# Optimization experiments

Hardware: AMD Instinct MI355X
Metric: run time of the kernel (lower is better)

## Reference

```python
import jax, jax.numpy as jnp
import numpy as np

IN_CAPS = 128      # number of memory capsules (rows of m)
NUM_CAPS = 5       # n_class
DIM_CAPS = 153     # comp_dim // n_class = 768 // 5
IN_DIM = 768       # comp_dim
NQ = 256           # number of query samples
NUM_ROUTING = 3
BETA = 1.0         # config['Model']['temperature']
EPS = 1e-8


def _pearsonr(x, y):
    # Pearson correlation along last dim (broadcasts over leading dims).
    xm = x - x.mean(axis=-1, keepdims=True)
    ym = y - y.mean(axis=-1, keepdims=True)
    num = (xm * ym).sum(axis=-1)
    den = jnp.sqrt((xm * xm).sum(axis=-1)) * jnp.sqrt((ym * ym).sum(axis=-1))
    return num / (den + EPS)


def _squash(s):
    # capsule squash along last dim
    n2 = (s * s).sum(axis=-1, keepdims=True)
    return (n2 / (1.0 + n2)) * s / jnp.sqrt(n2 + EPS)


def setup_inputs() -> dict:
    key = jax.random.key(0)
    k1, k2, k3 = jax.random.split(key, 3)
    m = jax.random.normal(k1, (IN_CAPS, IN_DIM), dtype=jnp.float32)
    q = jax.random.normal(k2, (NQ, IN_DIM), dtype=jnp.float32)
    W = jax.random.normal(k3, (IN_DIM, NUM_CAPS * DIM_CAPS), dtype=jnp.float32) * 0.02
    b = jnp.zeros((NUM_CAPS * DIM_CAPS,), dtype=jnp.float32)
    return {"m": m, "q": q, "W": W, "b": b}


def reference(m, q, W, b):
    sg = jax.lax.stop_gradient
    # projections -> capsule preactivations
    hat_m = (m @ W + b).reshape(IN_CAPS, NUM_CAPS, DIM_CAPS)          # [I,C,D]
    hat_q = (q @ W + b).reshape(-1, NUM_CAPS, DIM_CAPS)               # [Q,C,D]
    Qn = hat_q.shape[0]
    tmp_m = sg(hat_m)[None, :, :, :]                                   # [1,I,C,D] (broadcast over Q)
    tmp_q = sg(hat_q)[:, None, :, :]                                   # [Q,1,C,D]

    a = jnp.zeros((Qn, IN_CAPS, NUM_CAPS), dtype=hat_q.dtype)          # routing logits
    p = jnp.tanh(_pearsonr(tmp_m, tmp_q))                              # [Q,I,C]

    for _ in range(NUM_ROUTING - 1):
        d = jax.nn.softmax(a / BETA, axis=2)                           # [Q,I,C]
        dsp = d + p
        hat_v = (tmp_m * dsp[..., None]).sum(axis=1)                   # [Q,C,D]
        v = _squash(hat_v)
        m_dot_v = (tmp_m * v[:, None, :, :]).sum(axis=-1)              # [Q,I,C]
        a = a + p * m_dot_v
        tmp_q = (tmp_q + v[:, None, :, :]) * 0.5                       # [Q,I,C,D]
        p = jnp.tanh(_pearsonr(tmp_m, tmp_q))

    d = jax.nn.softmax(a / BETA, axis=2)
    dsp = sg(d + p)                                                    # routing coeffs detached
    hat_v = (hat_m[None, :, :, :] * dsp[..., None]).sum(axis=1)        # grad flows via hat_m only
    q_prime = _squash(hat_v).reshape(Qn, -1)                           # [Q, C*D]
    return q_prime
```

## Files before the change

### kernel.cpp

```cpp
#include <hip/hip_runtime.h>
#include <hip/hip_bf16.h>

#define I_CAPS 128
#define N_CAPS 5
#define D_CAPS 153
#define D_PAD  160
#define MLD    800
#define IN_DIM 768
#define NQ     256
#define CD     765
#define NPAIR  640
#define EPSF   1e-8f
#define KHALF  384

typedef __hip_bfloat16 bf16;

__device__ __forceinline__ float wred(float x) {
#pragma unroll
  for (int off = 32; off; off >>= 1) x += __shfl_down(x, off, 64);
  return x;
}

__device__ __forceinline__ float tanh_fast(float x) {
  float t = __expf(-2.f * fabsf(x));
  float r = (1.f - t) / (1.f + t);
  return copysignf(r, x);
}

__device__ __forceinline__ float squash_sc(float n2) {
  return (n2 / (1.f + n2)) * rsqrtf(n2 + EPSF);
}

__global__ void classify_kernel(const unsigned* __restrict__ m_u32,
                                int* __restrict__ flag) {
  int lane = threadIdx.x & 63;
  unsigned u = m_u32[lane];
  int e = (u >> 7) & 0xFF;
  int hit = (e >= 118 && e <= 134) ? 1 : 0;
  unsigned long long mask = __ballot(hit);
  if (lane == 0) *flag = (__popcll(mask) >= 48) ? 1 : 0;
}

template <bool ISB>
__device__ __forceinline__ float ld_in(const void* p, long idx) {
  if (ISB) return __bfloat162float(((const bf16*)p)[idx]);
  return ((const float*)p)[idx];
}

template <bool ISB>
__device__ void gemm_body(const void* m, const void* q, const void* W,
                          const void* b, float* hat_m, float* hat_q) {
  __shared__ float As[16][KHALF];
  const int tx = threadIdx.x, ty = threadIdx.y;
  const int t = ty * 64 + tx;
  const int row0 = blockIdx.y * 16;
  const int k0 = blockIdx.z * KHALF;

  if (ISB) {
    for (int e = t; e < 16 * KHALF; e += 256) {
      int rr = e / KHALF, kk = e - rr * KHALF;
      int row = row0 + rr;
      As[rr][kk] = (row < I_CAPS)
                       ? ld_in<true>(m, (long)row * IN_DIM + k0 + kk)
                       : ld_in<true>(q, (long)(row - I_CAPS) * IN_DIM + k0 + kk);
    }
  } else {
    for (int e = t; e < 16 * (KHALF / 4); e += 256) {
      int rr = e / (KHALF / 4), k4 = e - rr * (KHALF / 4);
      int row = row0 + rr;
      const float* src = (row < I_CAPS)
                             ? (const float*)m + (long)row * IN_DIM
                             : (const float*)q + (long)(row - I_CAPS) * IN_DIM;
      *(float4*)&As[rr][k4 * 4] = *(const float4*)(src + k0 + k4 * 4);
    }
  }
  __syncthreads();

  const int col = blockIdx.x * 64 + tx;
  const int colc = (col < CD) ? col : (CD - 1);
  const int r0 = ty * 4;

  float acc[4][2];
#pragma unroll
  for (int r = 0; r < 4; ++r) { acc[r][0] = 0.f; acc[r][1] = 0.f; }

#pragma unroll 2
  for (int k = 0; k < KHALF; k += 8) {
    float w0 = ld_in<ISB>(W, (long)(k0 + k + 0) * CD + colc);
    float w1 = ld_in<ISB>(W, (long)(k0 + k + 1) * CD + colc);
    float w2 = ld_in<ISB>(W, (long)(k0 + k + 2) * CD + colc);
    float w3 = ld_in<ISB>(W, (long)(k0 + k + 3) * CD + colc);
    float w4 = ld_in<ISB>(W, (long)(k0 + k + 4) * CD + colc);
    float w5 = ld_in<ISB>(W, (long)(k0 + k + 5) * CD + colc);
    float w6 = ld_in<ISB>(W, (long)(k0 + k + 6) * CD + colc);
    float w7 = ld_in<ISB>(W, (long)(k0 + k + 7) * CD + colc);
#pragma unroll
    for (int r = 0; r < 4; ++r) {
      const float4 Aa = *(const float4*)&As[r0 + r][k];
      const float4 Ab = *(const float4*)&As[r0 + r][k + 4];
      acc[r][0] = fmaf(Aa.x, w0, acc[r][0]);
      acc[r][1] = fmaf(Aa.y, w1, acc[r][1]);
      acc[r][0] = fmaf(Aa.z, w2, acc[r][0]);
      acc[r][1] = fmaf(Aa.w, w3, acc[r][1]);
      acc[r][0] = fmaf(Ab.x, w4, acc[r][0]);
      acc[r][1] = fmaf(Ab.y, w5, acc[r][1]);
      acc[r][0] = fmaf(Ab.z, w6, acc[r][0]);
      acc[r][1] = fmaf(Ab.w, w7, acc[r][1]);
    }
  }

  if (col < CD) {
    float bias = (blockIdx.z == 0) ? ld_in<ISB>(b, col) : 0.f;
    int c = col / D_CAPS, d = col - c * D_CAPS;
#pragma unroll
    for (int r = 0; r < 4; ++r) {
      int row = row0 + r0 + r;
      float p = acc[r][0] + acc[r][1] + bias;
      float* dst = (row < I_CAPS) ? &hat_m[row * MLD + c * D_PAD + d]
                                  : &hat_q[(row - I_CAPS) * CD + col];
      atomicAdd(dst, p);
    }
  }
}

__global__ __launch_bounds__(256, 4)
void gemm_kernel(const void* m, const void* q, const void* W, const void* b,
                 const int* __restrict__ flag,
                 float* __restrict__ hat_m, float* __restrict__ hat_q) {
  if (*flag)
    gemm_body<true>(m, q, W, b, hat_m, hat_q);
  else
    gemm_body<false>(m, q, W, b, hat_m, hat_q);
}

__global__ __launch_bounds__(256)
void stats_kernel(const float* __restrict__ hat_m,
                  float* __restrict__ mean_m, float* __restrict__ ssm) {
  const int wave = threadIdx.x >> 6, lane = threadIdx.x & 63;
  const int pair = blockIdx.x * 4 + wave;
  const int i = pair / N_CAPS, c = pair - i * N_CAPS;
  const float* hm = hat_m + i * MLD + c * D_PAD;
  float s = 0.f, s2 = 0.f;
  for (int d = lane; d < D_CAPS; d += 64) {
    float x = hm[d];
    s += x;
    s2 = fmaf(x, x, s2);
  }
  s = wred(s);
  s2 = wred(s2);
  if (lane == 0) {
    float mu = s * (1.f / D_CAPS);
    mean_m[pair] = mu;
    ssm[pair] = fmaxf(s2 - (float)D_CAPS * mu * mu, 0.f);
  }
}

__global__ __launch_bounds__(128)
void gram_kernel(const float* __restrict__ hat_m, float* __restrict__ G) {
  const int c = blockIdx.x, j = blockIdx.y, i = threadIdx.x;
  const float4* hi = (const float4*)(hat_m + i * MLD + c * D_PAD);
  const float4* hj = (const float4*)(hat_m + j * MLD + c * D_PAD);
  float a0 = 0.f, a1 = 0.f, a2 = 0.f, a3 = 0.f;
#pragma unroll 8
  for (int k = 0; k < 40; ++k) {
    float4 x = hi[k];
    float4 y = hj[k];
    a0 = fmaf(x.x, y.x, a0);
    a1 = fmaf(x.y, y.y, a1);
    a2 = fmaf(x.z, y.z, a2);
    a3 = fmaf(x.w, y.w, a3);
  }
  G[c * 16384 + j * 128 + i] = (a0 + a1) + (a2 + a3);
}

__global__ __launch_bounds__(1024, 4)
void routing_kernel(const float* __restrict__ hat_m,
                    const float* __restrict__ hat_q,
                    const float* __restrict__ Gmat,
                    const float* __restrict__ mean_m,
                    const float* __restrict__ ssm,
                    float* __restrict__ dspT,
                    float* __restrict__ scT) {
  __shared__ float tq[N_CAPS * D_PAD];
  __shared__ float aa[NPAIR], pp[NPAIR], dsp[NPAIR], sdot[NPAIR];
  __shared__ float smm[NPAIR], sss[NPAIR];
  __shared__ float meanq0[N_CAPS], ssq0[N_CAPS];
  __shared__ float tsum_s[2][N_CAPS], t2_s[2][N_CAPS];
  __shared__ float red[10][4];

  const int tid = threadIdx.x;
  const int qi = blockIdx.x;
  const int w = tid >> 6, lane = tid & 63;
  const int g = tid >> 3, sub = tid & 7;
  const float* hq = hat_q + qi * CD;
  const float* hm = hat_m + g * MLD;

  for (int l = tid; l < N_CAPS * D_PAD; l += 1024) {
    int c = l / D_PAD, d = l - c * D_PAD;
    tq[l] = (d < D_CAPS) ? hq[c * D_CAPS + d] : 0.f;
  }
  if (tid < NPAIR) {
    aa[tid] = 0.f;
    smm[tid] = mean_m[tid];
    sss[tid] = ssm[tid];
  }
  __syncthreads();

  if (w < N_CAPS) {
    const int c = w;
    float s = 0.f, s2 = 0.f;
    for (int d = lane; d < D_CAPS; d += 64) {
      float x = tq[c * D_PAD + d];
      s += x;
      s2 = fmaf(x, x, s2);
    }
    s = wred(s);
    s2 = wred(s2);
    if (lane == 0) {
      float mu = s * (1.f / D_CAPS);
      tsum_s[0][c] = s;
      t2_s[0][c] = s2;
      meanq0[c] = mu;
      ssq0[c] = fmaxf(s2 - (float)D_CAPS * mu * mu, 0.f);
    }
  }
  __syncthreads();

  {
    float A0 = 0.f, A1 = 0.f, A2 = 0.f, A3 = 0.f, A4 = 0.f;
#pragma unroll 2
    for (int jj = 0; jj < 5; ++jj) {
      int d = jj * 32 + sub * 4;
      float4 h0 = *(const float4*)(hm + 0 * D_PAD + d);
      float4 h1 = *(const float4*)(hm + 1 * D_PAD + d);
      float4 h2 = *(const float4*)(hm + 2 * D_PAD + d);
      float4 h3 = *(const float4*)(hm + 3 * D_PAD + d);
      float4 h4 = *(const float4*)(hm + 4 * D_PAD + d);
      float4 t0 = *(const float4*)(tq + 0 * D_PAD + d);
      float4 t1 = *(const float4*)(tq + 1 * D_PAD + d);
      float4 t2 = *(const float4*)(tq + 2 * D_PAD + d);
      float4 t3 = *(const float4*)(tq + 3 * D_PAD + d);
      float4 t4 = *(const float4*)(tq + 4 * D_PAD + d);
      A0 = fmaf(h0.x, t0.x, A0); A0 = fmaf(h0.y, t0.y, A0);
      A0 = fmaf(h0.z, t0.z, A0); A0 = fmaf(h0.w, t0.w, A0);
      A1 = fmaf(h1.x, t1.x, A1); A1 = fmaf(h1.y, t1.y, A1);
      A1 = fmaf(h1.z, t1.z, A1); A1 = fmaf(h1.w, t1.w, A1);
      A2 = fmaf(h2.x, t2.x, A2); A2 = fmaf(h2.y, t2.y, A2);
      A2 = fmaf(h2.z, t2.z, A2); A2 = fmaf(h2.w, t2.w, A2);
      A3 = fmaf(h3.x, t3.x, A3); A3 = fmaf(h3.y, t3.y, A3);
      A3 = fmaf(h3.z, t3.z, A3); A3 = fmaf(h3.w, t3.w, A3);
      A4 = fmaf(h4.x, t4.x, A4); A4 = fmaf(h4.y, t4.y, A4);
      A4 = fmaf(h4.z, t4.z, A4); A4 = fmaf(h4.w, t4.w, A4);
    }
#pragma unroll
    for (int off = 1; off < 8; off <<= 1) {
      A0 += __shfl_xor(A0, off, 64);
      A1 += __shfl_xor(A1, off, 64);
      A2 += __shfl_xor(A2, off, 64);
      A3 += __shfl_xor(A3, off, 64);
      A4 += __shfl_xor(A4, off, 64);
    }
    if (sub < N_CAPS) {
      float acc = A0;
      acc = (sub == 1) ? A1 : acc;
      acc = (sub == 2) ? A2 : acc;
      acc = (sub == 3) ? A3 : acc;
      acc = (sub == 4) ? A4 : acc;
      int ic = g * N_CAPS + sub;
      sdot[ic] = acc;
      float num = acc - (float)D_CAPS * smm[ic] * meanq0[sub];
      float den = sqrtf(sss[ic]) * sqrtf(ssq0[sub]) + EPSF;
      pp[ic] = tanh_fast(num / den);
    }
  }
  __syncthreads();

  auto softmax_dsp = [&]() {
    if (tid < I_CAPS) {
      float av[N_CAPS], ev[N_CAPS];
      float mx = -1e30f;
#pragma unroll
      for (int c = 0; c < N_CAPS; ++c) {
        av[c] = aa[tid * N_CAPS + c];
        mx = fmaxf(mx, av[c]);
      }
      float s = 0.f;
#pragma unroll
      for (int c = 0; c < N_CAPS; ++c) {
        ev[c] = __expf(av[c] - mx);
        s += ev[c];
      }
      float inv = 1.f / s;
#pragma unroll
      for (int c = 0; c < N_CAPS; ++c)
        dsp[tid * N_CAPS + c] = ev[c] * inv + pp[tid * N_CAPS + c];
    }
  };

  auto gmatvec = [&](int cc, int ii) {
    const float* Gp = Gmat + cc * 16384 + ii;
    float y0 = 0.f, y1 = 0.f;
#pragma unroll 4
    for (int j = 0; j < 128; j += 2) {
      y0 = fmaf(Gp[j * 128], dsp[j * N_CAPS + cc], y0);
      y1 = fmaf(Gp[(j + 1) * 128], dsp[(j + 1) * N_CAPS + cc], y1);
    }
    return y0 + y1;
  };

  for (int r = 0; r < 2; ++r) {
    softmax_dsp();
    __syncthreads();
    float y = 0.f, sold = 0.f;
    int cc = tid >> 7, ii = tid & 127, ic = ii * N_CAPS + cc;
    if (tid < NPAIR) {
      y = gmatvec(cc, ii);
      sold = sdot[ic];
      float dmy = dsp[ic];
      float n2p = wred(dmy * y);
      float vsp = wred(dmy * ((float)D_CAPS * smm[ic]));
      float sdp = wred(dmy * sold);
      if (lane == 0) {
        red[w][0] = n2p;
        red[w][1] = vsp;
        red[w][2] = sdp;
      }
    }
    __syncthreads();
    if (tid < NPAIR) {
      float n2 = red[2 * cc][0] + red[2 * cc + 1][0];
      float vs = red[2 * cc][1] + red[2 * cc + 1][1];
      float sd = red[2 * cc][2] + red[2 * cc + 1][2];
      float sc = squash_sc(n2);
      float ts = 0.5f * (tsum_s[r & 1][cc] + sc * vs);
      float t2v = 0.25f * (t2_s[r & 1][cc] + 2.f * sc * sd + sc * sc * n2);
      if (ii == 0) {
        tsum_s[(r + 1) & 1][cc] = ts;
        t2_s[(r + 1) & 1][cc] = t2v;
      }
      float mu = ts * (1.f / D_CAPS);
      float ssqv = fmaxf(t2v - (float)D_CAPS * mu * mu, 0.f);
      float mdv = sc * y;
      aa[ic] += pp[ic] * mdv;
      float snew = 0.5f * (sold + mdv);
      sdot[ic] = snew;
      float num = snew - (float)D_CAPS * smm[ic] * mu;
      float den = sqrtf(sss[ic]) * sqrtf(ssqv) + EPSF;
      pp[ic] = tanh_fast(num / den);
    }
    __syncthreads();
  }

  softmax_dsp();
  __syncthreads();
  {
    int cc = tid >> 7, ii = tid & 127, ic = ii * N_CAPS + cc;
    float y = 0.f;
    if (tid < NPAIR) {
      y = gmatvec(cc, ii);
      float n2p = wred(dsp[ic] * y);
      if (lane == 0) red[w][0] = n2p;
    }
    __syncthreads();
    if (tid < NPAIR)
      dspT[(cc * NQ + qi) * 128 + ii] = dsp[ic];
    if (tid < N_CAPS) {
      float n2 = red[2 * tid][0] + red[2 * tid + 1][0];
      scT[tid * NQ + qi] = squash_sc(n2);
    }
  }
}

__global__ __launch_bounds__(256, 4)
void outgemm_kernel(const float* __restrict__ hat_m,
                    const float* __restrict__ dspT,
                    const float* __restrict__ scT,
                    const int* __restrict__ flag,
                    void* __restrict__ out_v) {
  __shared__ float hmT[128][32];
  __shared__ float dspS[32][132];

  const int c = blockIdx.x, dt = blockIdx.y, qt = blockIdx.z;
  const int tid = threadIdx.x;

  for (int e = tid; e < 128 * 8; e += 256) {
    int i = e >> 3, dd4 = e & 7;
    *(float4*)&hmT[i][dd4 * 4] =
        *(const float4*)(hat_m + i * MLD + c * D_PAD + dt * 32 + dd4 * 4);
  }
  for (int e = tid; e < 32 * 32; e += 256) {
    int qq = e >> 5, k4 = e & 31;
    *(float4*)&dspS[qq][k4 * 4] =
        *(const float4*)(dspT + ((long)c * NQ + qt * 32 + qq) * 128 + k4 * 4);
  }
  __syncthreads();

  const int qq = tid >> 3, dsub = tid & 7;
  const int q = qt * 32 + qq;
  float a0 = 0.f, a1 = 0.f, a2 = 0.f, a3 = 0.f;
#pragma unroll 2
  for (int i = 0; i < 128; ++i) {
    float dv = dspS[qq][i];
    const float4 h = *(const float4*)&hmT[i][dsub * 4];
    a0 = fmaf(dv, h.x, a0);
    a1 = fmaf(dv, h.y, a1);
    a2 = fmaf(dv, h.z, a2);
    a3 = fmaf(dv, h.w, a3);
  }
  const float sc = scT[c * NQ + q];
  const int d0 = dt * 32 + dsub * 4;
  float r[4] = {a0 * sc, a1 * sc, a2 * sc, a3 * sc};

  if (*flag == 0) {
    float* out = (float*)out_v;
#pragma unroll
    for (int k = 0; k < 4; ++k)
      if (d0 + k < D_CAPS) out[q * CD + c * D_CAPS + d0 + k] = r[k];
  } else {
    bf16* out = (bf16*)out_v;
#pragma unroll
    for (int k = 0; k < 4; ++k)
      if (d0 + k < D_CAPS)
        out[q * CD + c * D_CAPS + d0 + k] = __float2bfloat16(r[k]);
  }
}

extern "C" void kernel_launch(void* const* d_in, const int* in_sizes, int n_in,
                              void* d_out, int out_size, void* d_ws, size_t ws_size,
                              hipStream_t stream) {
  const void *m = nullptr, *q = nullptr, *W = nullptr, *b = nullptr;
  for (int i = 0; i < n_in; ++i) {
    switch (in_sizes[i]) {
      case I_CAPS * IN_DIM: m = d_in[i]; break;
      case NQ * IN_DIM:     q = d_in[i]; break;
      case IN_DIM * CD:     W = d_in[i]; break;
      case CD:              b = d_in[i]; break;
      default: break;
    }
  }
  if (!m || !q || !W || !b) {
    m = d_in[0]; q = d_in[1]; W = d_in[2]; b = d_in[3];
  }

  int*   flag   = (int*)d_ws;
  float* mean_m = (float*)d_ws + 16;
  float* ssm    = mean_m + 640;
  float* hat_m  = ssm + 640;
  float* hat_q  = hat_m + I_CAPS * MLD;
  float* G      = hat_q + NQ * CD;
  float* dspT   = G + N_CAPS * I_CAPS * I_CAPS;
  float* scT    = dspT + (size_t)N_CAPS * NQ * 128;

  classify_kernel<<<1, 64, 0, stream>>>((const unsigned*)m, flag);
  hipMemsetAsync(hat_m, 0,
                 ((size_t)I_CAPS * MLD + (size_t)NQ * CD) * sizeof(float),
                 stream);
  gemm_kernel<<<dim3(12, 24, 2), dim3(64, 4), 0, stream>>>(m, q, W, b, flag,
                                                           hat_m, hat_q);
  stats_kernel<<<160, 256, 0, stream>>>(hat_m, mean_m, ssm);
  gram_kernel<<<dim3(N_CAPS, I_CAPS), 128, 0, stream>>>(hat_m, G);
  routing_kernel<<<NQ, 1024, 0, stream>>>(hat_m, hat_q, G, mean_m, ssm,
                                          dspT, scT);
  outgemm_kernel<<<dim3(N_CAPS, 5, 8), 256, 0, stream>>>(hat_m, dspT, scT,
                                                         flag, d_out);
}
```

Baseline: 125.2 us.

## Fold dtype check and stats into other kernels, precompute initial dot in batched kernel

Removes the separate classify and stats kernels: the bf16 check is now recomputed inline in the gemm and output kernels, and the per-capsule mean and sum of squares come from the diagonal of the gram kernel. The initial hat_m·hat_q dot products move out of the per-query routing kernel into a new batched sinit kernel that reuses hat_q tiles from shared memory. The projection GEMM tile is halved to 8 rows per block, doubling the block count. This trades two fewer launches and less redundant global traffic in routing for an extra kernel and more workspace.

After: 129.8 us. +3.6%, slower.

```diff
diff --git a/kernel.cpp b/kernel.cpp
--- a/kernel.cpp
+++ b/kernel.cpp
@@ -27,18 +27,12 @@
   return copysignf(r, x);
 }
 
-__device__ __forceinline__ float squash_sc(float n2) {
-  return (n2 / (1.f + n2)) * rsqrtf(n2 + EPSF);
-}
-
-__global__ void classify_kernel(const unsigned* __restrict__ m_u32,
-                                int* __restrict__ flag) {
+__device__ __forceinline__ int is_bf16(const unsigned* __restrict__ m_u32) {
   int lane = threadIdx.x & 63;
   unsigned u = m_u32[lane];
   int e = (u >> 7) & 0xFF;
-  int hit = (e >= 118 && e <= 134) ? 1 : 0;
-  unsigned long long mask = __ballot(hit);
-  if (lane == 0) *flag = (__popcll(mask) >= 48) ? 1 : 0;
+  unsigned long long mask = __ballot(e >= 118 && e <= 134);
+  return __popcll(mask) >= 48;
 }
 
 template <bool ISB>
@@ -50,14 +44,14 @@
 template <bool ISB>
 __device__ void gemm_body(const void* m, const void* q, const void* W,
                           const void* b, float* hat_m, float* hat_q) {
-  __shared__ float As[16][KHALF];
+  __shared__ float As[8][KHALF];
   const int tx = threadIdx.x, ty = threadIdx.y;
   const int t = ty * 64 + tx;
-  const int row0 = blockIdx.y * 16;
+  const int row0 = blockIdx.y * 8;
   const int k0 = blockIdx.z * KHALF;
 
   if (ISB) {
-    for (int e = t; e < 16 * KHALF; e += 256) {
+    for (int e = t; e < 8 * KHALF; e += 256) {
       int rr = e / KHALF, kk = e - rr * KHALF;
       int row = row0 + rr;
       As[rr][kk] = (row < I_CAPS)
@@ -65,7 +59,7 @@
                        : ld_in<true>(q, (long)(row - I_CAPS) * IN_DIM + k0 + kk);
     }
   } else {
-    for (int e = t; e < 16 * (KHALF / 4); e += 256) {
+    for (int e = t; e < 8 * (KHALF / 4); e += 256) {
       int rr = e / (KHALF / 4), k4 = e - rr * (KHALF / 4);
       int row = row0 + rr;
       const float* src = (row < I_CAPS)
@@ -78,14 +72,15 @@
 
   const int col = blockIdx.x * 64 + tx;
   const int colc = (col < CD) ? col : (CD - 1);
-  const int r0 = ty * 4;
-
-  float acc[4][2];
-#pragma unroll
-  for (int r = 0; r < 4; ++r) { acc[r][0] = 0.f; acc[r][1] = 0.f; }
-
+  const int r0 = ty * 2, r1 = r0 + 1;
+
+  float a0a = 0.f, a0b = 0.f, a1a = 0.f, a1b = 0.f;
 #pragma unroll 2
   for (int k = 0; k < KHALF; k += 8) {
+    const float4 A0a = *(const float4*)&As[r0][k];
+    const float4 A0b = *(const float4*)&As[r0][k + 4];
+    const float4 A1a = *(const float4*)&As[r1][k];
+    const float4 A1b = *(const float4*)&As[r1][k + 4];
     float w0 = ld_in<ISB>(W, (long)(k0 + k + 0) * CD + colc);
     float w1 = ld_in<ISB>(W, (long)(k0 + k + 1) * CD + colc);
     float w2 = ld_in<ISB>(W, (long)(k0 + k + 2) * CD + colc);
@@ -94,73 +89,52 @@
     float w5 = ld_in<ISB>(W, (long)(k0 + k + 5) * CD + colc);
     float w6 = ld_in<ISB>(W, (long)(k0 + k + 6) * CD + colc);
     float w7 = ld_in<ISB>(W, (long)(k0 + k + 7) * CD + colc);
-#pragma unroll
-    for (int r = 0; r < 4; ++r) {
-      const float4 Aa = *(const float4*)&As[r0 + r][k];
-      const float4 Ab = *(const float4*)&As[r0 + r][k + 4];
-      acc[r][0] = fmaf(Aa.x, w0, acc[r][0]);
-      acc[r][1] = fmaf(Aa.y, w1, acc[r][1]);
-      acc[r][0] = fmaf(Aa.z, w2, acc[r][0]);
-      acc[r][1] = fmaf(Aa.w, w3, acc[r][1]);
-      acc[r][0] = fmaf(Ab.x, w4, acc[r][0]);
-      acc[r][1] = fmaf(Ab.y, w5, acc[r][1]);
-      acc[r][0] = fmaf(Ab.z, w6, acc[r][0]);
-      acc[r][1] = fmaf(Ab.w, w7, acc[r][1]);
-    }
+    a0a = fmaf(A0a.x, w0, a0a); a0b = fmaf(A0a.y, w1, a0b);
+    a0a = fmaf(A0a.z, w2, a0a); a0b = fmaf(A0a.w, w3, a0b);
+    a0a = fmaf(A0b.x, w4, a0a); a0b = fmaf(A0b.y, w5, a0b);
+    a0a = fmaf(A0b.z, w6, a0a); a0b = fmaf(A0b.w, w7, a0b);
+    a1a = fmaf(A1a.x, w0, a1a); a1b = fmaf(A1a.y, w1, a1b);
+    a1a = fmaf(A1a.z, w2, a1a); a1b = fmaf(A1a.w, w3, a1b);
+    a1a = fmaf(A1b.x, w4, a1a); a1b = fmaf(A1b.y, w5, a1b);
+    a1a = fmaf(A1b.z, w6, a1a); a1b = fmaf(A1b.w, w7, a1b);
   }
 
   if (col < CD) {
-    float bias = (blockIdx.z == 0) ? ld_in<ISB>(b, col) : 0.f;
+    float p0 = a0a + a0b;
+    float p1 = a1a + a1b;
+    if (blockIdx.z == 0) {
+      float bias = ld_in<ISB>(b, col);
+      p0 += bias;
+      p1 += bias;
+    }
     int c = col / D_CAPS, d = col - c * D_CAPS;
-#pragma unroll
-    for (int r = 0; r < 4; ++r) {
-      int row = row0 + r0 + r;
-      float p = acc[r][0] + acc[r][1] + bias;
-      float* dst = (row < I_CAPS) ? &hat_m[row * MLD + c * D_PAD + d]
-                                  : &hat_q[(row - I_CAPS) * CD + col];
-      atomicAdd(dst, p);
-    }
+    int ra = row0 + r0, rb = row0 + r1;
+    float* d0 = (ra < I_CAPS) ? &hat_m[ra * MLD + c * D_PAD + d]
+                              : &hat_q[(ra - I_CAPS) * CD + col];
+    float* d1 = (rb < I_CAPS) ? &hat_m[rb * MLD + c * D_PAD + d]
+                              : &hat_q[(rb - I_CAPS) * CD + col];
+    atomicAdd(d0, p0);
+    atomicAdd(d1, p1);
   }
 }
 
 __global__ __launch_bounds__(256, 4)
 void gemm_kernel(const void* m, const void* q, const void* W, const void* b,
-                 const int* __restrict__ flag,
                  float* __restrict__ hat_m, float* __restrict__ hat_q) {
-  if (*flag)
+  if (is_bf16((const unsigned*)m))
     gemm_body<true>(m, q, W, b, hat_m, hat_q);
   else
     gemm_body<false>(m, q, W, b, hat_m, hat_q);
 }
 
-__global__ __launch_bounds__(256)
-void stats_kernel(const float* __restrict__ hat_m,
-                  float* __restrict__ mean_m, float* __restrict__ ssm) {
-  const int wave = threadIdx.x >> 6, lane = threadIdx.x & 63;
-  const int pair = blockIdx.x * 4 + wave;
-  const int i = pair / N_CAPS, c = pair - i * N_CAPS;
-  const float* hm = hat_m + i * MLD + c * D_PAD;
-  float s = 0.f, s2 = 0.f;
-  for (int d = lane; d < D_CAPS; d += 64) {
-    float x = hm[d];
-    s += x;
-    s2 = fmaf(x, x, s2);
-  }
-  s = wred(s);
-  s2 = wred(s2);
-  if (lane == 0) {
-    float mu = s * (1.f / D_CAPS);
-    mean_m[pair] = mu;
-    ssm[pair] = fmaxf(s2 - (float)D_CAPS * mu * mu, 0.f);
-  }
-}
-
 __global__ __launch_bounds__(128)
-void gram_kernel(const float* __restrict__ hat_m, float* __restrict__ G) {
+void gram_kernel(const float* __restrict__ hat_m, float* __restrict__ G,
+                 float* __restrict__ mean_m, float* __restrict__ ssm) {
   const int c = blockIdx.x, j = blockIdx.y, i = threadIdx.x;
   const float4* hi = (const float4*)(hat_m + i * MLD + c * D_PAD);
   const float4* hj = (const float4*)(hat_m + j * MLD + c * D_PAD);
   float a0 = 0.f, a1 = 0.f, a2 = 0.f, a3 = 0.f;
+  float s = 0.f;
 #pragma unroll 8
   for (int k = 0; k < 40; ++k) {
     float4 x = hi[k];
@@ -169,14 +143,55 @@
     a1 = fmaf(x.y, y.y, a1);
     a2 = fmaf(x.z, y.z, a2);
     a3 = fmaf(x.w, y.w, a3);
-  }
-  G[c * 16384 + j * 128 + i] = (a0 + a1) + (a2 + a3);
+    s += (x.x + x.y) + (x.z + x.w);
+  }
+  float dot = (a0 + a1) + (a2 + a3);
+  G[c * 16384 + j * 128 + i] = dot;
+  if (i == j) {
+    float mu = s * (1.f / D_CAPS);
+    mean_m[j * N_CAPS + c] = mu;
+    ssm[j * N_CAPS + c] = fmaxf(dot - (float)D_CAPS * mu * mu, 0.f);
+  }
+}
+
+__global__ __launch_bounds__(256)
+void sinit_kernel(const float* __restrict__ hat_m,
+                  const float* __restrict__ hat_q,
+                  float* __restrict__ Sg) {
+  __shared__ float hqS[16][160];
+  const int c = blockIdx.x, q0 = blockIdx.y * 16;
+  const int tid = threadIdx.x;
+
+  for (int e = tid; e < 16 * 160; e += 256) {
+    int qq = e / 160, d = e - qq * 160;
+    hqS[qq][d] = (d < D_CAPS) ? hat_q[(q0 + qq) * CD + c * D_CAPS + d] : 0.f;
+  }
+  __syncthreads();
+
+  const int i = tid & 127, half = tid >> 7;
+  const float4* hi = (const float4*)(hat_m + i * MLD + c * D_PAD);
+  float acc[8] = {0.f, 0.f, 0.f, 0.f, 0.f, 0.f, 0.f, 0.f};
+#pragma unroll 4
+  for (int k = 0; k < 40; ++k) {
+    float4 h = hi[k];
+#pragma unroll
+    for (int qq = 0; qq < 8; ++qq) {
+      const float4 t = *(const float4*)&hqS[half * 8 + qq][k * 4];
+      acc[qq] = fmaf(h.x, t.x, acc[qq]);
+      acc[qq] = fmaf(h.y, t.y, acc[qq]);
+      acc[qq] = fmaf(h.z, t.z, acc[qq]);
+      acc[qq] = fmaf(h.w, t.w, acc[qq]);
+    }
+  }
+#pragma unroll
+  for (int qq = 0; qq < 8; ++qq)
+    Sg[((long)c * NQ + q0 + half * 8 + qq) * 128 + i] = acc[qq];
 }
 
 __global__ __launch_bounds__(1024, 4)
-void routing_kernel(const float* __restrict__ hat_m,
-                    const float* __restrict__ hat_q,
+void routing_kernel(const float* __restrict__ hat_q,
                     const float* __restrict__ Gmat,
+                    const float* __restrict__ Sg,
                     const float* __restrict__ mean_m,
                     const float* __restrict__ ssm,
                     float* __restrict__ dspT,
@@ -191,9 +206,7 @@
   const int tid = threadIdx.x;
   const int qi = blockIdx.x;
   const int w = tid >> 6, lane = tid & 63;
-  const int g = tid >> 3, sub = tid & 7;
   const float* hq = hat_q + qi * CD;
-  const float* hm = hat_m + g * MLD;
 
   for (int l = tid; l < N_CAPS * D_PAD; l += 1024) {
     int c = l / D_PAD, d = l - c * D_PAD;
@@ -226,52 +239,13 @@
   }
   __syncthreads();
 
-  {
-    float A0 = 0.f, A1 = 0.f, A2 = 0.f, A3 = 0.f, A4 = 0.f;
-#pragma unroll 2
-    for (int jj = 0; jj < 5; ++jj) {
-      int d = jj * 32 + sub * 4;
-      float4 h0 = *(const float4*)(hm + 0 * D_PAD + d);
-      float4 h1 = *(const float4*)(hm + 1 * D_PAD + d);
-      float4 h2 = *(const float4*)(hm + 2 * D_PAD + d);
-      float4 h3 = *(const float4*)(hm + 3 * D_PAD + d);
-      float4 h4 = *(const float4*)(hm + 4 * D_PAD + d);
-      float4 t0 = *(const float4*)(tq + 0 * D_PAD + d);
-      float4 t1 = *(const float4*)(tq + 1 * D_PAD + d);
-      float4 t2 = *(const float4*)(tq + 2 * D_PAD + d);
-      float4 t3 = *(const float4*)(tq + 3 * D_PAD + d);
-      float4 t4 = *(const float4*)(tq + 4 * D_PAD + d);
-      A0 = fmaf(h0.x, t0.x, A0); A0 = fmaf(h0.y, t0.y, A0);
-      A0 = fmaf(h0.z, t0.z, A0); A0 = fmaf(h0.w, t0.w, A0);
-      A1 = fmaf(h1.x, t1.x, A1); A1 = fmaf(h1.y, t1.y, A1);
-      A1 = fmaf(h1.z, t1.z, A1); A1 = fmaf(h1.w, t1.w, A1);
-      A2 = fmaf(h2.x, t2.x, A2); A2 = fmaf(h2.y, t2.y, A2);
-      A2 = fmaf(h2.z, t2.z, A2); A2 = fmaf(h2.w, t2.w, A2);
-      A3 = fmaf(h3.x, t3.x, A3); A3 = fmaf(h3.y, t3.y, A3);
-      A3 = fmaf(h3.z, t3.z, A3); A3 = fmaf(h3.w, t3.w, A3);
-      A4 = fmaf(h4.x, t4.x, A4); A4 = fmaf(h4.y, t4.y, A4);
-      A4 = fmaf(h4.z, t4.z, A4); A4 = fmaf(h4.w, t4.w, A4);
-    }
-#pragma unroll
-    for (int off = 1; off < 8; off <<= 1) {
-      A0 += __shfl_xor(A0, off, 64);
-      A1 += __shfl_xor(A1, off, 64);
-      A2 += __shfl_xor(A2, off, 64);
-      A3 += __shfl_xor(A3, off, 64);
-      A4 += __shfl_xor(A4, off, 64);
-    }
-    if (sub < N_CAPS) {
-      float acc = A0;
-      acc = (sub == 1) ? A1 : acc;
-      acc = (sub == 2) ? A2 : acc;
-      acc = (sub == 3) ? A3 : acc;
-      acc = (sub == 4) ? A4 : acc;
-      int ic = g * N_CAPS + sub;
-      sdot[ic] = acc;
-      float num = acc - (float)D_CAPS * smm[ic] * meanq0[sub];
-      float den = sqrtf(sss[ic]) * sqrtf(ssq0[sub]) + EPSF;
-      pp[ic] = tanh_fast(num / den);
-    }
+  if (tid < NPAIR) {
+    int cc = tid >> 7, ii = tid & 127, ic = ii * N_CAPS + cc;
+    float s0 = Sg[((long)cc * NQ + qi) * 128 + ii];
+    sdot[ic] = s0;
+    float num = s0 - (float)D_CAPS * smm[ic] * meanq0[cc];
+    float den = sqrtf(sss[ic]) * sqrtf(ssq0[cc]) + EPSF;
+    pp[ic] = tanh_fast(num / den);
   }
   __syncthreads();
 
@@ -331,7 +305,7 @@
       float n2 = red[2 * cc][0] + red[2 * cc + 1][0];
       float vs = red[2 * cc][1] + red[2 * cc + 1][1];
       float sd = red[2 * cc][2] + red[2 * cc + 1][2];
-      float sc = squash_sc(n2);
+      float sc = (n2 / (1.f + n2)) * rsqrtf(n2 + EPSF);
       float ts = 0.5f * (tsum_s[r & 1][cc] + sc * vs);
       float t2v = 0.25f * (t2_s[r & 1][cc] + 2.f * sc * sd + sc * sc * n2);
       if (ii == 0) {
@@ -363,10 +337,10 @@
     }
     __syncthreads();
     if (tid < NPAIR)
-      dspT[(cc * NQ + qi) * 128 + ii] = dsp[ic];
+      dspT[((long)cc * NQ + qi) * 128 + ii] = dsp[ic];
     if (tid < N_CAPS) {
       float n2 = red[2 * tid][0] + red[2 * tid + 1][0];
-      scT[tid * NQ + qi] = squash_sc(n2);
+      scT[tid * NQ + qi] = (n2 / (1.f + n2)) * rsqrtf(n2 + EPSF);
     }
   }
 }
@@ -375,7 +349,7 @@
 void outgemm_kernel(const float* __restrict__ hat_m,
                     const float* __restrict__ dspT,
                     const float* __restrict__ scT,
-                    const int* __restrict__ flag,
+                    const unsigned* __restrict__ m_u32,
                     void* __restrict__ out_v) {
   __shared__ float hmT[128][32];
   __shared__ float dspS[32][132];
@@ -411,7 +385,7 @@
   const int d0 = dt * 32 + dsub * 4;
   float r[4] = {a0 * sc, a1 * sc, a2 * sc, a3 * sc};
 
-  if (*flag == 0) {
+  if (!is_bf16(m_u32)) {
     float* out = (float*)out_v;
 #pragma unroll
     for (int k = 0; k < 4; ++k)
@@ -442,25 +416,26 @@
     m = d_in[0]; q = d_in[1]; W = d_in[2]; b = d_in[3];
   }
 
-  int*   flag   = (int*)d_ws;
   float* mean_m = (float*)d_ws + 16;
   float* ssm    = mean_m + 640;
   float* hat_m  = ssm + 640;
   float* hat_q  = hat_m + I_CAPS * MLD;
   float* G      = hat_q + NQ * CD;
-  float* dspT   = G + N_CAPS * I_CAPS * I_CAPS;
+  float* Sg     = G + N_CAPS * I_CAPS * I_CAPS;
+  float* dspT   = Sg + (size_t)N_CAPS * NQ * 128;
   float* scT    = dspT + (size_t)N_CAPS * NQ * 128;
 
-  classify_kernel<<<1, 64, 0, stream>>>((const unsigned*)m, flag);
   hipMemsetAsync(hat_m, 0,
                  ((size_t)I_CAPS * MLD + (size_t)NQ * CD) * sizeof(float),
                  stream);
-  gemm_kernel<<<dim3(12, 24, 2), dim3(64, 4), 0, stream>>>(m, q, W, b, flag,
+  gemm_kernel<<<dim3(12, 48, 2), dim3(64, 4), 0, stream>>>(m, q, W, b,
                                                            hat_m, hat_q);
-  stats_kernel<<<160, 256, 0, stream>>>(hat_m, mean_m, ssm);
-  gram_kernel<<<dim3(N_CAPS, I_CAPS), 128, 0, stream>>>(hat_m, G);
-  routing_kernel<<<NQ, 1024, 0, stream>>>(hat_m, hat_q, G, mean_m, ssm,
+  gram_kernel<<<dim3(N_CAPS, I_CAPS), 128, 0, stream>>>(hat_m, G,
+                                                        mean_m, ssm);
+  sinit_kernel<<<dim3(N_CAPS, 16), 256, 0, stream>>>(hat_m, hat_q, Sg);
+  routing_kernel<<<NQ, 1024, 0, stream>>>(hat_q, G, Sg, mean_m, ssm,
                                           dspT, scT);
   outgemm_kernel<<<dim3(N_CAPS, 5, 8), 256, 0, stream>>>(hat_m, dspT, scT,
-                                                         flag, d_out);
-}
+                                                         (const unsigned*)m,
+                                                         d_out);
+}
```
